# Optimization experiments

Measured on AMD Instinct MI355X. Metric: run time of the kernel, lower is better.

The kernel has to match this reference:

```python
import jax, jax.numpy as jnp
import numpy as np

N_NODES = 50000
N_EDGES = 800000
X_DIM, EDGE_DIM, H_DIM, HOUT = 92, 80, 128, 128
N_CONV = 3
N_GRAPHS = 256
BN_EPS = 1e-5


def setup_inputs() -> dict:
    key = jax.random.key(0)
    ks = jax.random.split(key, 16)
    x = jax.random.normal(ks[0], (N_NODES, X_DIM), dtype=jnp.float32)
    edge_index = jax.random.randint(ks[1], (2, N_EDGES), 0, N_NODES, dtype=jnp.int64)
    edge_attr = jax.random.normal(ks[2], (N_EDGES, EDGE_DIM), dtype=jnp.float32)
    batch = jnp.sort(jax.random.randint(ks[3], (N_NODES,), 0, N_GRAPHS, dtype=jnp.int64))
    s = 0.05
    embed_W = jax.random.normal(ks[4], (X_DIM, H_DIM), dtype=jnp.float32) * s
    embed_b = jnp.zeros((H_DIM,), jnp.float32)
    in_dim = 2 * H_DIM + EDGE_DIM
    conv_W = jax.random.normal(ks[5], (N_CONV, in_dim, 2 * H_DIM), dtype=jnp.float32) * s
    conv_b = jnp.zeros((N_CONV, 2 * H_DIM), jnp.float32)
    bn_i_g = jnp.ones((N_CONV, 2 * H_DIM), jnp.float32)
    bn_i_b = jnp.zeros((N_CONV, 2 * H_DIM), jnp.float32)
    bn_o_g = jnp.ones((N_CONV, H_DIM), jnp.float32)
    bn_o_b = jnp.zeros((N_CONV, H_DIM), jnp.float32)
    lin_W = jax.random.normal(ks[6], (H_DIM, HOUT), dtype=jnp.float32) * s
    lin_b = jnp.zeros((HOUT,), jnp.float32)
    out_W = jax.random.normal(ks[7], (HOUT, 1), dtype=jnp.float32) * s
    out_b = jnp.zeros((1,), jnp.float32)
    return {"x": x, "edge_index": edge_index, "edge_attr": edge_attr, "batch": batch,
            "embed_W": embed_W, "embed_b": embed_b, "conv_W": conv_W, "conv_b": conv_b,
            "bn_i_g": bn_i_g, "bn_i_b": bn_i_b, "bn_o_g": bn_o_g, "bn_o_b": bn_o_b,
            "lin_W": lin_W, "lin_b": lin_b, "out_W": out_W, "out_b": out_b}


def _bn(h, gamma, beta):
    # training-mode BatchNorm1d: biased batch statistics
    mu = jnp.mean(h, axis=0)
    var = jnp.mean(jnp.square(h - mu), axis=0)
    return (h - mu) * jax.lax.rsqrt(var + BN_EPS) * gamma + beta


def _cgconv(x, edge_index, edge_attr, W, b, gi, bi, go, bo):
    src, dst = edge_index[0], edge_index[1]
    msg = jnp.concatenate([x[src], edge_attr, x[dst]], axis=1)  # [E, 2h+e]
    msg = msg @ W + b                                           # [E, 2h]
    msg = _bn(msg, gi, bi)
    filt, core = jnp.split(msg, 2, axis=1)
    gated = jax.nn.sigmoid(filt) * jax.nn.softplus(core)        # [E, h]
    agg = jax.ops.segment_sum(gated, src, num_segments=N_NODES)  # [N, h]
    agg = _bn(agg, go, bo)
    return jax.nn.softplus(x + agg)


def reference(x, edge_index, edge_attr, batch, embed_W, embed_b, conv_W, conv_b,
              bn_i_g, bn_i_b, bn_o_g, bn_o_b, lin_W, lin_b, out_W, out_b):
    h = x @ embed_W + embed_b  # [N, h_dim]
    for i in range(N_CONV):
        h = _cgconv(h, edge_index, edge_attr, conv_W[i], conv_b[i],
                    bn_i_g[i], bn_i_b[i], bn_o_g[i], bn_o_b[i])
    # mean pooling per graph
    sums = jax.ops.segment_sum(h, batch, num_segments=N_GRAPHS)
    cnts = jax.ops.segment_sum(jnp.ones((h.shape[0],), h.dtype), batch, num_segments=N_GRAPHS)
    pooled = sums / jnp.maximum(cnts, 1.0)[:, None]  # [G, h_dim]
    g = jax.nn.softplus(pooled @ lin_W + lin_b)
    return g @ out_W + out_b  # [G, 1]
```

## Files before the change

kernel.cpp:

```cpp
#include <hip/hip_runtime.h>

constexpr int NN = 50000;
constexpr int NE = 800000;
constexpr int XD = 92;
constexpr int ED = 80;
constexpr int HD = 128;
constexpr int C2 = 256;
constexpr int IND = 336;
constexpr int NC = 3;
constexpr int NG = 256;
constexpr int NTILES = NE / 64;
constexpr int WSZ_L = 16 * 3 * 64 * 8;
constexpr int WNP_L = 16 * 4 * 64 * 8;

#define DINL __device__ __forceinline__

typedef __attribute__((ext_vector_type(8))) short bf16x8;
typedef __attribute__((ext_vector_type(4))) float f32x4;

DINL short f2bf(float f) {
  unsigned u = __float_as_uint(f);
  u = (u + 0x7fffu + ((u >> 16) & 1u)) >> 16;
  return (short)u;
}
DINL float bf2f(unsigned short u) { return __uint_as_float(((unsigned)u) << 16); }
DINL float bflo(unsigned u) { return __uint_as_float(u << 16); }
DINL float bfhi(unsigned u) { return __uint_as_float(u & 0xffff0000u); }
DINL float rcp_(float x) {
  float r;
  asm("v_rcp_f32 %0, %1" : "=v"(r) : "v"(x));
  return r;
}
DINL float softplusf_(float x) { return x > 20.f ? x : log1pf(__expf(x)); }
DINL float gate_(float f, float cr) {
  float e = __expf(-f);
  float s = rcp_(1.f + e);
  float t = __expf(cr);
  float l = (cr > 15.f) ? cr : __logf(1.f + t);
  return s * l;
}

template <int CTRL>
DINL int dpp_i(int old_, int src) {
  return __builtin_amdgcn_update_dpp(old_, src, CTRL, 0xF, 0xF, false);
}
template <int CTRL>
DINL float dpp_f(float old_, float src) {
  return __int_as_float(
      __builtin_amdgcn_update_dpp(__float_as_int(old_), __float_as_int(src), CTRL, 0xF, 0xF, false));
}
constexpr int SHR1 = 0x111, SHR2 = 0x112, SHR4 = 0x114, SHR8 = 0x118, SHL1 = 0x101;

__global__ __launch_bounds__(256) void k_embed(const float* __restrict__ x,
    const float* __restrict__ W, const float* __restrict__ b, float* __restrict__ h,
    unsigned short* __restrict__ hbf) {
  __shared__ float xs[2][XD];
  int t = threadIdx.x;
  int n0 = blockIdx.x * 2;
  for (int i = t; i < 2 * XD; i += 256) xs[i / XD][i % XD] = x[(size_t)n0 * XD + i];
  __syncthreads();
  int lo = t >> 7, c = t & 127;
  float acc = b[c];
  for (int k = 0; k < XD; ++k) acc = fmaf(xs[lo][k], W[k * HD + c], acc);
  h[(size_t)(n0 + lo) * HD + c] = acc;
  hbf[(size_t)(n0 + lo) * HD + c] = (unsigned short)f2bf(acc);
}

__global__ __launch_bounds__(256) void k_hist(const int* __restrict__ src,
                                              int* __restrict__ deg) {
  for (int e = blockIdx.x * 256 + threadIdx.x; e < NE; e += gridDim.x * 256)
    atomicAdd(&deg[src[e]], 1);
}

__global__ __launch_bounds__(1024) void k_scan(const int* __restrict__ deg,
                                               int* __restrict__ cursor) {
  __shared__ int sums[1024];
  int t = threadIdx.x;
  const int CH = 49;
  int b0 = t * CH;
  int s = 0;
  for (int i = 0; i < CH; ++i) {
    int idx = b0 + i;
    if (idx < NN) s += deg[idx];
  }
  sums[t] = s;
  __syncthreads();
  for (int off = 1; off < 1024; off <<= 1) {
    int v = (t >= off) ? sums[t - off] : 0;
    __syncthreads();
    sums[t] += v;
    __syncthreads();
  }
  int excl = (t == 0) ? 0 : sums[t - 1];
  for (int i = 0; i < CH; ++i) {
    int idx = b0 + i;
    if (idx < NN) {
      cursor[idx] = excl;
      excl += deg[idx];
    }
  }
}

__global__ __launch_bounds__(256) void k_scatter(const int* __restrict__ src,
    const int* __restrict__ dst, int* __restrict__ cursor, int* __restrict__ eid,
    int* __restrict__ ssort, int* __restrict__ dsort) {
  for (int e = blockIdx.x * 256 + threadIdx.x; e < NE; e += gridDim.x * 256) {
    int s = src[e];
    int pos = atomicAdd(&cursor[s], 1);
    eid[pos] = e;
    ssort[pos] = s;
    dsort[pos] = dst[e];
  }
}

__global__ __launch_bounds__(256) void k_wprep(const float* __restrict__ convW,
                                               unsigned short* __restrict__ Wswz) {
  int idx = blockIdx.x * 256 + threadIdx.x;
  if (idx >= NC * WSZ_L) return;
  int L = idx / WSZ_L;
  int rem = idx - L * WSZ_L;
  int mt = rem / 1536;
  int rem2 = rem - mt * 1536;
  int ks = rem2 >> 9;
  int lane = (rem2 >> 3) & 63;
  int j = rem2 & 7;
  int k = ks * 32 + (lane >> 4) * 8 + j;
  int m = mt * 16 + (lane & 15);
  float v = (k < ED) ? convW[(size_t)L * IND * C2 + (size_t)(HD + k) * C2 + m] : 0.f;
  Wswz[idx] = (unsigned short)f2bf(v);
}

__global__ __launch_bounds__(256) void k_wprep2(const float* __restrict__ convW,
                                                unsigned short* __restrict__ Wn) {
  int idx = blockIdx.x * 256 + threadIdx.x;
  if (idx >= NC * 2 * WNP_L) return;
  int Lh = idx >> 15;
  int L = Lh >> 1, half = Lh & 1;
  int rem = idx & 32767;
  int mt = rem >> 11;
  int rem2 = rem & 2047;
  int ks = rem2 >> 9;
  int lane = (rem2 >> 3) & 63;
  int j = rem2 & 7;
  int k = ks * 32 + (lane >> 4) * 8 + j;
  int m = mt * 16 + (lane & 15);
  int row = (half ? 208 : 0) + k;
  Wn[idx] = (unsigned short)f2bf(convW[(size_t)L * IND * C2 + (size_t)row * C2 + m]);
}

__global__ __launch_bounds__(256) void k_nodeproj2(const unsigned short* __restrict__ hbf,
    const unsigned short* __restrict__ Wn, int L,
    ushort4* __restrict__ P1, ushort4* __restrict__ P3) {
  __shared__ bf16x8 hls[1024];
  __shared__ ushort4 outls[4096];
  int t = threadIdx.x, w = t >> 6, l = t & 63, g = l >> 4, c = l & 15;
  int n0 = blockIdx.x * 64;
  int half = blockIdx.y;
  for (int i = t; i < 1024; i += 256) {
    int node = i >> 4, chunk = i & 15;
    int gn = n0 + node;
    if (gn >= NN) gn = NN - 1;
    bf16x8 v = *(const bf16x8*)(hbf + (size_t)gn * HD + chunk * 8);
    hls[node * 16 + (chunk ^ (node & 7))] = v;
  }
  __syncthreads();
  const bf16x8* Wf = (const bf16x8*)(Wn + ((size_t)(L * 2 + half)) * WNP_L);
  bf16x8 af[4][4];
#pragma unroll
  for (int mm = 0; mm < 4; ++mm)
#pragma unroll
    for (int ks = 0; ks < 4; ++ks) af[mm][ks] = Wf[((w * 4 + mm) * 4 + ks) * 64 + l];
  f32x4 acc[4][4];
#pragma unroll
  for (int mm = 0; mm < 4; ++mm)
#pragma unroll
    for (int nt = 0; nt < 4; ++nt)
#pragma unroll
      for (int i = 0; i < 4; ++i) acc[mm][nt][i] = 0.f;
#pragma unroll
  for (int nt = 0; nt < 4; ++nt) {
    int node = nt * 16 + c;
#pragma unroll
    for (int ks = 0; ks < 4; ++ks) {
      bf16x8 b = hls[node * 16 + ((4 * ks + g) ^ (node & 7))];
#pragma unroll
      for (int mm = 0; mm < 4; ++mm)
        acc[mm][nt] = __builtin_amdgcn_mfma_f32_16x16x32_bf16(af[mm][ks], b, acc[mm][nt], 0, 0, 0);
    }
  }
  __syncthreads();
#pragma unroll
  for (int mm = 0; mm < 4; ++mm) {
    int mt = w * 4 + mm;
    int wE = (mt & 7) >> 1;
    int mE = (mt & 1) | ((mt >> 3) << 1);
    int slot = (wE * 4 + g) * 4 + mE;
#pragma unroll
    for (int nt = 0; nt < 4; ++nt) {
      int node = nt * 16 + c;
      ushort4 st;
      st.x = (unsigned short)f2bf(acc[mm][nt][0]);
      st.y = (unsigned short)f2bf(acc[mm][nt][1]);
      st.z = (unsigned short)f2bf(acc[mm][nt][2]);
      st.w = (unsigned short)f2bf(acc[mm][nt][3]);
      outls[node * 64 + (slot ^ ((node & 7) << 3))] = st;
    }
  }
  __syncthreads();
  ushort4* P = half ? P3 : P1;
  for (int i = t; i < 4096; i += 256) {
    int row = i >> 6, slot = i & 63;
    int gn = n0 + row;
    if (gn < NN) P[(size_t)gn * 64 + slot] = outls[row * 64 + (slot ^ ((row & 7) << 3))];
  }
}

__global__ __launch_bounds__(256) void k_eaprep(const int* __restrict__ eid,
    const float* __restrict__ ea, bf16x8* __restrict__ eaf) {
  int idx = blockIdx.x * 256 + threadIdx.x;
  if (idx >= NTILES * 768) return;
  int tile = idx / 768;
  int r = idx - tile * 768;
  int fr = r >> 6, l = r & 63;
  int nt = fr / 3, ks = fr - 3 * nt;
  int c = l & 15, g = l >> 4;
  int k0 = ks * 32 + g * 8;
  bf16x8 v;
  if (k0 < ED) {
    int e = eid[tile * 64 + nt * 16 + c];
    const float* p = ea + (size_t)e * ED + k0;
    float4 x0 = *(const float4*)p;
    float4 x1 = *(const float4*)(p + 4);
    v[0] = f2bf(x0.x); v[1] = f2bf(x0.y); v[2] = f2bf(x0.z); v[3] = f2bf(x0.w);
    v[4] = f2bf(x1.x); v[5] = f2bf(x1.y); v[6] = f2bf(x1.z); v[7] = f2bf(x1.w);
  } else {
#pragma unroll
    for (int j = 0; j < 8; ++j) v[j] = 0;
  }
  eaf[idx] = v;
}

__global__ __launch_bounds__(256, 2) void k_estat2(
    const int* __restrict__ ssort, const int* __restrict__ dsort,
    const bf16x8* __restrict__ eaf, const unsigned short* __restrict__ Wswz,
    const uint4* __restrict__ P1p, const uint4* __restrict__ P3p,
    ushort4* __restrict__ msgc, float* __restrict__ stats) {
  int t = threadIdx.x;
  int w = t >> 6, l = t & 63;
  int g = l >> 4, c = l & 15;
  int mtg[4] = {2 * w, 2 * w + 1, 2 * w + 8, 2 * w + 9};
  int gi2 = (w * 4 + g) * 2;
  const bf16x8* Wf = (const bf16x8*)Wswz;
  bf16x8 af[4][3];
#pragma unroll
  for (int m = 0; m < 4; ++m)
#pragma unroll
    for (int ks = 0; ks < 3; ++ks) af[m][ks] = Wf[(mtg[m] * 3 + ks) * 64 + l];
  f32x4 ssum[4], ssq[4];
#pragma unroll
  for (int m = 0; m < 4; ++m)
#pragma unroll
    for (int i = 0; i < 4; ++i) { ssum[m][i] = 0.f; ssq[m][i] = 0.f; }

  const int stride = gridDim.x;
  int tile = blockIdx.x;
  int s_[4], d_[4];
  if (tile < NTILES) {
#pragma unroll
    for (int nt = 0; nt < 4; ++nt) {
      s_[nt] = ssort[tile * 64 + nt * 16 + c];
      d_[nt] = dsort[tile * 64 + nt * 16 + c];
    }
  }
  for (; tile < NTILES; tile += stride) {
    bf16x8 b_[12];
    const bf16x8* bp = eaf + (size_t)tile * 768 + l;
#pragma unroll
    for (int fr = 0; fr < 12; ++fr) b_[fr] = bp[fr * 64];
    uint4 q1a[4], q1b[4], q3a[4], q3b[4];
#pragma unroll
    for (int nt = 0; nt < 4; ++nt) {
      const uint4* p1 = P1p + (size_t)s_[nt] * 32 + gi2;
      const uint4* p3 = P3p + (size_t)d_[nt] * 32 + gi2;
      q1a[nt] = p1[0];
      q1b[nt] = p1[1];
      q3a[nt] = p3[0];
      q3b[nt] = p3[1];
    }
    int sn[4], dn[4];
    int tn = tile + stride;
    if (tn < NTILES) {
#pragma unroll
      for (int nt = 0; nt < 4; ++nt) {
        sn[nt] = ssort[tn * 64 + nt * 16 + c];
        dn[nt] = dsort[tn * 64 + nt * 16 + c];
      }
    } else {
#pragma unroll
      for (int nt = 0; nt < 4; ++nt) { sn[nt] = 0; dn[nt] = 0; }
    }
#pragma unroll
    for (int nt = 0; nt < 4; ++nt) {
      f32x4 acc[4];
#pragma unroll
      for (int m = 0; m < 4; ++m) {
        acc[m][0] = 0.f; acc[m][1] = 0.f; acc[m][2] = 0.f; acc[m][3] = 0.f;
      }
#pragma unroll
      for (int ks = 0; ks < 3; ++ks)
#pragma unroll
        for (int m = 0; m < 4; ++m)
          acc[m] = __builtin_amdgcn_mfma_f32_16x16x32_bf16(af[m][ks], b_[nt * 3 + ks],
                                                           acc[m], 0, 0, 0);
      unsigned pu1[8] = {q1a[nt].x, q1a[nt].y, q1a[nt].z, q1a[nt].w,
                         q1b[nt].x, q1b[nt].y, q1b[nt].z, q1b[nt].w};
      unsigned pu3[8] = {q3a[nt].x, q3a[nt].y, q3a[nt].z, q3a[nt].w,
                         q3b[nt].x, q3b[nt].y, q3b[nt].z, q3b[nt].w};
#pragma unroll
      for (int m = 0; m < 4; ++m) {
        unsigned a1 = pu1[2 * m], b1 = pu1[2 * m + 1];
        unsigned a3 = pu3[2 * m], b3 = pu3[2 * m + 1];
        f32x4 ms;
        ms[0] = acc[m][0] + bflo(a1) + bflo(a3);
        ms[1] = acc[m][1] + bfhi(a1) + bfhi(a3);
        ms[2] = acc[m][2] + bflo(b1) + bflo(b3);
        ms[3] = acc[m][3] + bfhi(b1) + bfhi(b3);
#pragma unroll
        for (int i = 0; i < 4; ++i) {
          ssum[m][i] += ms[i];
          ssq[m][i] = fmaf(ms[i], ms[i], ssq[m][i]);
        }
        ushort4 st;
        st.x = (unsigned short)f2bf(ms[0]);
        st.y = (unsigned short)f2bf(ms[1]);
        st.z = (unsigned short)f2bf(ms[2]);
        st.w = (unsigned short)f2bf(ms[3]);
        msgc[(((size_t)tile * 4 + nt) * 16 + w * 4 + m) * 64 + l] = st;
      }
    }
#pragma unroll
    for (int nt = 0; nt < 4; ++nt) { s_[nt] = sn[nt]; d_[nt] = dn[nt]; }
  }
#pragma unroll
  for (int off = 1; off < 16; off <<= 1)
#pragma unroll
    for (int m = 0; m < 4; ++m)
#pragma unroll
      for (int i = 0; i < 4; ++i) {
        ssum[m][i] += __shfl_xor(ssum[m][i], off, 16);
        ssq[m][i] += __shfl_xor(ssq[m][i], off, 16);
      }
  if (c == 0) {
#pragma unroll
    for (int m = 0; m < 4; ++m)
#pragma unroll
      for (int i = 0; i < 4; ++i) {
        int ch = mtg[m] * 16 + 4 * g + i;
        atomicAdd(&stats[ch], ssum[m][i]);
        atomicAdd(&stats[C2 + ch], ssq[m][i]);
      }
  }
}

__global__ __launch_bounds__(256) void k_apply2(
    const int* __restrict__ ssort, const ushort4* __restrict__ msgc,
    const float* __restrict__ st, const float* __restrict__ gammaI,
    const float* __restrict__ betaI, float* __restrict__ agg) {
  int t = threadIdx.x;
  int w = t >> 6, l = t & 63;
  int g = l >> 4, c = l & 15;
  int mtg[4] = {2 * w, 2 * w + 1, 2 * w + 8, 2 * w + 9};
  f32x4 sc4[4], sh4[4];
#pragma unroll
  for (int m = 0; m < 4; ++m)
#pragma unroll
    for (int i = 0; i < 4; ++i) {
      int ch = mtg[m] * 16 + 4 * g + i;
      float mean = st[ch] * (1.f / NE);
      float var = st[C2 + ch] * (1.f / NE) - mean * mean;
      float scv = gammaI[ch] * rsqrtf(var + 1e-5f);
      sc4[m][i] = scv;
      sh4[m][i] = betaI[ch] - mean * scv;
    }
  const int stride = gridDim.x;
  int tile = blockIdx.x;
  if (tile >= NTILES) return;
  int s_[4];
  ushort4 mw[4][4];
#pragma unroll
  for (int nt = 0; nt < 4; ++nt) {
    s_[nt] = ssort[tile * 64 + nt * 16 + c];
#pragma unroll
    for (int m = 0; m < 4; ++m)
      mw[nt][m] = msgc[(((size_t)tile * 4 + nt) * 16 + w * 4 + m) * 64 + l];
  }
  for (; tile < NTILES; tile += stride) {
    int tn = tile + stride;
    int ti = (tn < NTILES) ? tn : tile;
    int sn[4];
    ushort4 mwn[4][4];
#pragma unroll
    for (int nt = 0; nt < 4; ++nt) {
      sn[nt] = ssort[ti * 64 + nt * 16 + c];
#pragma unroll
      for (int m = 0; m < 4; ++m)
        mwn[nt][m] = msgc[(((size_t)ti * 4 + nt) * 16 + w * 4 + m) * 64 + l];
    }
#pragma unroll
    for (int nt = 0; nt < 4; ++nt) {
      int sv = s_[nt];
      int ps = dpp_i<SHR1>(-1, sv);
      int hp = (ps != sv) ? c : 0;
      hp = max(hp, dpp_i<SHR1>(0, hp));
      hp = max(hp, dpp_i<SHR2>(0, hp));
      hp = max(hp, dpp_i<SHR4>(0, hp));
      hp = max(hp, dpp_i<SHR8>(0, hp));
      int ns = dpp_i<SHL1>(-1, sv);
      bool tail = (ns != sv);
      bool g1 = (c - 1) >= hp, g2 = (c - 2) >= hp, g4 = (c - 4) >= hp, g8 = (c - 8) >= hp;
      f32x4 v4[4];
#pragma unroll
      for (int m = 0; m < 4; ++m) {
        v4[m][0] = fmaf(bf2f(mw[nt][m].x), sc4[m][0], sh4[m][0]);
        v4[m][1] = fmaf(bf2f(mw[nt][m].y), sc4[m][1], sh4[m][1]);
        v4[m][2] = fmaf(bf2f(mw[nt][m].z), sc4[m][2], sh4[m][2]);
        v4[m][3] = fmaf(bf2f(mw[nt][m].w), sc4[m][3], sh4[m][3]);
      }
      float gg_[8];
#pragma unroll
      for (int p = 0; p < 2; ++p)
#pragma unroll
        for (int i = 0; i < 4; ++i)
          gg_[p * 4 + i] = gate_(v4[p][i], v4[p + 2][i]);
#pragma unroll
      for (int q = 0; q < 8; ++q) {
        float tv;
        tv = dpp_f<SHR1>(0.f, gg_[q]); gg_[q] += g1 ? tv : 0.f;
        tv = dpp_f<SHR2>(0.f, gg_[q]); gg_[q] += g2 ? tv : 0.f;
        tv = dpp_f<SHR4>(0.f, gg_[q]); gg_[q] += g4 ? tv : 0.f;
        tv = dpp_f<SHR8>(0.f, gg_[q]); gg_[q] += g8 ? tv : 0.f;
      }
      if (tail) {
#pragma unroll
        for (int p = 0; p < 2; ++p)
#pragma unroll
          for (int i = 0; i < 4; ++i)
            atomicAdd(&agg[(size_t)sv * HD + mtg[p] * 16 + 4 * g + i], gg_[p * 4 + i]);
      }
    }
#pragma unroll
    for (int nt = 0; nt < 4; ++nt) {
      s_[nt] = sn[nt];
#pragma unroll
      for (int m = 0; m < 4; ++m) mw[nt][m] = mwn[nt][m];
    }
  }
}

__global__ __launch_bounds__(256) void k_aggstat(const float* __restrict__ agg,
                                                 float* __restrict__ stats) {
  int t = threadIdx.x;
  int c = t & 127, half = t >> 7;
  float s = 0.f, sq = 0.f;
  for (int n = blockIdx.x * 2 + half; n < NN; n += gridDim.x * 2) {
    float v = agg[(size_t)n * HD + c];
    s += v;
    sq = fmaf(v, v, sq);
  }
  __shared__ float shs[2][128], shq[2][128];
  shs[half][c] = s;
  shq[half][c] = sq;
  __syncthreads();
  if (t < 128) {
    atomicAdd(&stats[c], shs[0][c] + shs[1][c]);
    atomicAdd(&stats[128 + c], shq[0][c] + shq[1][c]);
  }
}

__global__ __launch_bounds__(256) void k_update(const float* __restrict__ h,
    const float* __restrict__ agg, const float* __restrict__ st_o,
    const float* __restrict__ bog, const float* __restrict__ bob,
    float* __restrict__ hn, unsigned short* __restrict__ hbf) {
  int stride = gridDim.x * 256;
  for (int i = blockIdx.x * 256 + threadIdx.x; i < NN * HD; i += stride) {
    int c = i & 127;
    float mean = st_o[c] * (1.f / NN);
    float var = st_o[128 + c] * (1.f / NN) - mean * mean;
    float scv = bog[c] * rsqrtf(var + 1e-5f);
    float shv = bob[c] - mean * scv;
    float v = h[i] + fmaf(agg[i], scv, shv);
    float r = softplusf_(v);
    hn[i] = r;
    hbf[i] = (unsigned short)f2bf(r);
  }
}

__global__ __launch_bounds__(256) void k_pool(const float* __restrict__ h,
    const int* __restrict__ batch, float* __restrict__ psum, int* __restrict__ pcnt) {
  int stride = gridDim.x * 256;
  for (int i = blockIdx.x * 256 + threadIdx.x; i < NN * HD; i += stride) {
    int n = i >> 7, c = i & 127;
    int g = batch[n];
    atomicAdd(&psum[g * HD + c], h[i]);
    if (c == 0) atomicAdd(&pcnt[g], 1);
  }
}

__global__ __launch_bounds__(128) void k_head(const float* __restrict__ psum,
    const int* __restrict__ pcnt, const float* __restrict__ linW,
    const float* __restrict__ linb, const float* __restrict__ outW,
    const float* __restrict__ outb, float* __restrict__ out) {
  __shared__ float pl[HD];
  __shared__ float red[2];
  int g = blockIdx.x, t = threadIdx.x;
  float cnt = fmaxf((float)pcnt[g], 1.f);
  pl[t] = psum[g * HD + t] / cnt;
  __syncthreads();
  float acc = linb[t];
  for (int k = 0; k < HD; ++k) acc = fmaf(pl[k], linW[k * HD + t], acc);
  float term = softplusf_(acc) * outW[t];
#pragma unroll
  for (int off = 32; off > 0; off >>= 1) term += __shfl_down(term, off, 64);
  if ((t & 63) == 0) red[t >> 6] = term;
  __syncthreads();
  if (t == 0) out[g] = red[0] + red[1] + outb[0];
}

extern "C" void kernel_launch(void* const* d_in, const int* in_sizes, int n_in,
                              void* d_out, int out_size, void* d_ws, size_t ws_size,
                              hipStream_t stream) {
  const float* x = (const float*)d_in[0];
  const int* ei = (const int*)d_in[1];
  const float* ea = (const float*)d_in[2];
  const int* batch = (const int*)d_in[3];
  const float* embW = (const float*)d_in[4];
  const float* embb = (const float*)d_in[5];
  const float* convW = (const float*)d_in[6];
  const float* big = (const float*)d_in[8];
  const float* bib = (const float*)d_in[9];
  const float* bog = (const float*)d_in[10];
  const float* bob = (const float*)d_in[11];
  const float* linW = (const float*)d_in[12];
  const float* linb = (const float*)d_in[13];
  const float* outW = (const float*)d_in[14];
  const float* outb = (const float*)d_in[15];
  float* out = (float*)d_out;

  float* wsf = (float*)d_ws;
  size_t off = 0;
  auto alloc = [&](size_t n) {
    float* p = wsf + off;
    off += (n + 3) & ~(size_t)3;
    return p;
  };
  float* h0 = alloc((size_t)NN * HD);
  float* h1 = alloc((size_t)NN * HD);
  unsigned short* hbf = (unsigned short*)alloc((size_t)NN * HD / 2);
  ushort4* P1b = (ushort4*)alloc((size_t)NN * C2 / 2);
  ushort4* P3b = (ushort4*)alloc((size_t)NN * C2 / 2);
  float* agg = alloc((size_t)NN * HD);
  float* st_i = alloc(2 * C2);
  float* st_o = alloc(2 * HD);
  float* psum = alloc((size_t)NG * HD);
  int* pcnt = (int*)alloc(NG);
  int* deg = (int*)alloc(NN);
  int* cursor = (int*)alloc(NN);
  int* eid = (int*)alloc(NE);
  int* ssort = (int*)alloc(NE);
  int* dsort = (int*)alloc(NE);
  unsigned short* Wswz = (unsigned short*)alloc((NC * WSZ_L + 1) / 2);
  unsigned short* Wn = (unsigned short*)alloc((NC * 2 * WNP_L + 1) / 2);
  bf16x8* eaf = (bf16x8*)alloc((size_t)NTILES * 768 * 4);
  ushort4* msgc = (ushort4*)alloc((size_t)NE * C2 / 2);

  const int* srcp = ei;
  const int* dstp = ei + NE;

  hipMemsetAsync(deg, 0, NN * sizeof(int), stream);
  k_hist<<<2048, 256, 0, stream>>>(srcp, deg);
  k_scan<<<1, 1024, 0, stream>>>(deg, cursor);
  k_scatter<<<2048, 256, 0, stream>>>(srcp, dstp, cursor, eid, ssort, dsort);

  k_wprep<<<(NC * WSZ_L + 255) / 256, 256, 0, stream>>>(convW, Wswz);
  k_wprep2<<<(NC * 2 * WNP_L + 255) / 256, 256, 0, stream>>>(convW, Wn);
  k_eaprep<<<(NTILES * 768 + 255) / 256, 256, 0, stream>>>(eid, ea, eaf);
  k_embed<<<NN / 2, 256, 0, stream>>>(x, embW, embb, h0, hbf);

  float* hc = h0;
  float* hn = h1;
  for (int L = 0; L < NC; ++L) {
    const unsigned short* Wl = Wswz + (size_t)L * WSZ_L;
    hipMemsetAsync(st_i, 0, 2 * C2 * sizeof(float), stream);
    hipMemsetAsync(st_o, 0, 2 * HD * sizeof(float), stream);
    hipMemsetAsync(agg, 0, (size_t)NN * HD * sizeof(float), stream);

    dim3 npgrid((NN + 63) / 64, 2);
    k_nodeproj2<<<npgrid, 256, 0, stream>>>(hbf, Wn, L, P1b, P3b);
    k_estat2<<<2500, 256, 0, stream>>>(ssort, dsort, eaf, Wl,
        (const uint4*)P1b, (const uint4*)P3b, msgc, st_i);
    k_apply2<<<2500, 256, 0, stream>>>(ssort, msgc, st_i, big + L * C2, bib + L * C2, agg);
    k_aggstat<<<512, 256, 0, stream>>>(agg, st_o);
    k_update<<<2048, 256, 0, stream>>>(hc, agg, st_o, bog + L * HD, bob + L * HD, hn, hbf);
    float* tmp = hc; hc = hn; hn = tmp;
  }

  hipMemsetAsync(psum, 0, (size_t)NG * HD * sizeof(float), stream);
  hipMemsetAsync(pcnt, 0, NG * sizeof(int), stream);
  k_pool<<<2048, 256, 0, stream>>>(hc, batch, psum, pcnt);
  k_head<<<NG, 128, 0, stream>>>(psum, pcnt, linW, linb, outW, outb, out);
}
```

Before: 2.236 ms.

## Split edge-stat kernel work into half-channel units across twice as many blocks

```diff
diff --git a/kernel.cpp b/kernel.cpp
--- a/kernel.cpp
+++ b/kernel.cpp
@@ -248,76 +248,70 @@
   int t = threadIdx.x;
   int w = t >> 6, l = t & 63;
   int g = l >> 4, c = l & 15;
-  int mtg[4] = {2 * w, 2 * w + 1, 2 * w + 8, 2 * w + 9};
-  int gi2 = (w * 4 + g) * 2;
+  const int stride = gridDim.x;
+  int unit = blockIdx.x;
+  int h = unit & 1;
+  int mtg[2] = {2 * w + 8 * h, 2 * w + 1 + 8 * h};
+  int giq = (w * 4 + g) * 2 + h;
   const bf16x8* Wf = (const bf16x8*)Wswz;
-  bf16x8 af[4][3];
-#pragma unroll
-  for (int m = 0; m < 4; ++m)
+  bf16x8 af[2][3];
+#pragma unroll
+  for (int m = 0; m < 2; ++m)
 #pragma unroll
     for (int ks = 0; ks < 3; ++ks) af[m][ks] = Wf[(mtg[m] * 3 + ks) * 64 + l];
-  f32x4 ssum[4], ssq[4];
-#pragma unroll
-  for (int m = 0; m < 4; ++m)
+  f32x4 ssum[2], ssq[2];
+#pragma unroll
+  for (int m = 0; m < 2; ++m)
 #pragma unroll
     for (int i = 0; i < 4; ++i) { ssum[m][i] = 0.f; ssq[m][i] = 0.f; }
 
-  const int stride = gridDim.x;
-  int tile = blockIdx.x;
+  const int NUNITS = 2 * NTILES;
   int s_[4], d_[4];
-  if (tile < NTILES) {
-#pragma unroll
-    for (int nt = 0; nt < 4; ++nt) {
-      s_[nt] = ssort[tile * 64 + nt * 16 + c];
-      d_[nt] = dsort[tile * 64 + nt * 16 + c];
-    }
-  }
-  for (; tile < NTILES; tile += stride) {
+  {
+    int tile0 = unit >> 1;
+#pragma unroll
+    for (int nt = 0; nt < 4; ++nt) {
+      s_[nt] = ssort[tile0 * 64 + nt * 16 + c];
+      d_[nt] = dsort[tile0 * 64 + nt * 16 + c];
+    }
+  }
+  for (; unit < NUNITS; unit += stride) {
+    int tile = unit >> 1;
     bf16x8 b_[12];
     const bf16x8* bp = eaf + (size_t)tile * 768 + l;
 #pragma unroll
     for (int fr = 0; fr < 12; ++fr) b_[fr] = bp[fr * 64];
-    uint4 q1a[4], q1b[4], q3a[4], q3b[4];
-#pragma unroll
-    for (int nt = 0; nt < 4; ++nt) {
-      const uint4* p1 = P1p + (size_t)s_[nt] * 32 + gi2;
-      const uint4* p3 = P3p + (size_t)d_[nt] * 32 + gi2;
-      q1a[nt] = p1[0];
-      q1b[nt] = p1[1];
-      q3a[nt] = p3[0];
-      q3b[nt] = p3[1];
+    uint4 q1[4], q3[4];
+#pragma unroll
+    for (int nt = 0; nt < 4; ++nt) {
+      q1[nt] = P1p[(size_t)s_[nt] * 32 + giq];
+      q3[nt] = P3p[(size_t)d_[nt] * 32 + giq];
     }
     int sn[4], dn[4];
-    int tn = tile + stride;
-    if (tn < NTILES) {
-#pragma unroll
-      for (int nt = 0; nt < 4; ++nt) {
-        sn[nt] = ssort[tn * 64 + nt * 16 + c];
-        dn[nt] = dsort[tn * 64 + nt * 16 + c];
-      }
-    } else {
-#pragma unroll
-      for (int nt = 0; nt < 4; ++nt) { sn[nt] = 0; dn[nt] = 0; }
-    }
-#pragma unroll
-    for (int nt = 0; nt < 4; ++nt) {
-      f32x4 acc[4];
-#pragma unroll
-      for (int m = 0; m < 4; ++m) {
+    int un = unit + stride;
+    int tin = (un < NUNITS) ? (un >> 1) : (unit >> 1);
+#pragma unroll
+    for (int nt = 0; nt < 4; ++nt) {
+      sn[nt] = ssort[tin * 64 + nt * 16 + c];
+      dn[nt] = dsort[tin * 64 + nt * 16 + c];
+    }
+#pragma unroll
+    for (int nt = 0; nt < 4; ++nt) {
+      f32x4 acc[2];
+#pragma unroll
+      for (int m = 0; m < 2; ++m) {
         acc[m][0] = 0.f; acc[m][1] = 0.f; acc[m][2] = 0.f; acc[m][3] = 0.f;
       }
 #pragma unroll
       for (int ks = 0; ks < 3; ++ks)
 #pragma unroll
-        for (int m = 0; m < 4; ++m)
+        for (int m = 0; m < 2; ++m)
           acc[m] = __builtin_amdgcn_mfma_f32_16x16x32_bf16(af[m][ks], b_[nt * 3 + ks],
                                                            acc[m], 0, 0, 0);
-      unsigned pu1[8] = {q1a[nt].x, q1a[nt].y, q1a[nt].z, q1a[nt].w,
-                         q1b[nt].x, q1b[nt].y, q1b[nt].z, q1b[nt].w};
-      unsigned pu3[8] = {q3a[nt].x, q3a[nt].y, q3a[nt].z, q3a[nt].w,
-                         q3b[nt].x, q3b[nt].y, q3b[nt].z, q3b[nt].w};
-#pragma unroll
-      for (int m = 0; m < 4; ++m) {
+      unsigned pu1[4] = {q1[nt].x, q1[nt].y, q1[nt].z, q1[nt].w};
+      unsigned pu3[4] = {q3[nt].x, q3[nt].y, q3[nt].z, q3[nt].w};
+#pragma unroll
+      for (int m = 0; m < 2; ++m) {
         unsigned a1 = pu1[2 * m], b1 = pu1[2 * m + 1];
         unsigned a3 = pu3[2 * m], b3 = pu3[2 * m + 1];
         f32x4 ms;
@@ -335,7 +329,7 @@
         st.y = (unsigned short)f2bf(ms[1]);
         st.z = (unsigned short)f2bf(ms[2]);
         st.w = (unsigned short)f2bf(ms[3]);
-        msgc[(((size_t)tile * 4 + nt) * 16 + w * 4 + m) * 64 + l] = st;
+        msgc[(((size_t)tile * 4 + nt) * 16 + w * 4 + 2 * h + m) * 64 + l] = st;
       }
     }
 #pragma unroll
@@ -344,7 +338,7 @@
 #pragma unroll
   for (int off = 1; off < 16; off <<= 1)
 #pragma unroll
-    for (int m = 0; m < 4; ++m)
+    for (int m = 0; m < 2; ++m)
 #pragma unroll
       for (int i = 0; i < 4; ++i) {
         ssum[m][i] += __shfl_xor(ssum[m][i], off, 16);
@@ -352,7 +346,7 @@
       }
   if (c == 0) {
 #pragma unroll
-    for (int m = 0; m < 4; ++m)
+    for (int m = 0; m < 2; ++m)
 #pragma unroll
       for (int i = 0; i < 4; ++i) {
         int ch = mtg[m] * 16 + 4 * g + i;
@@ -596,7 +590,7 @@
 
     dim3 npgrid((NN + 63) / 64, 2);
     k_nodeproj2<<<npgrid, 256, 0, stream>>>(hbf, Wn, L, P1b, P3b);
-    k_estat2<<<2500, 256, 0, stream>>>(ssort, dsort, eaf, Wl,
+    k_estat2<<<5000, 256, 0, stream>>>(ssort, dsort, eaf, Wl,
         (const uint4*)P1b, (const uint4*)P3b, msgc, st_i);
     k_apply2<<<2500, 256, 0, stream>>>(ssort, msgc, st_i, big + L * C2, bib + L * C2, agg);
     k_aggstat<<<512, 256, 0, stream>>>(agg, st_o);
```

Measured after the change: 2.462 ms. 1.1x slower.

## Recompute edge messages in apply pass instead of storing bf16 intermediate

Applied to the files above, without the earlier changes.

```diff
diff --git a/kernel.cpp b/kernel.cpp
--- a/kernel.cpp
+++ b/kernel.cpp
@@ -240,11 +240,11 @@
   eaf[idx] = v;
 }
 
-__global__ __launch_bounds__(256, 2) void k_estat2(
+__global__ __launch_bounds__(256, 2) void k_estat3(
     const int* __restrict__ ssort, const int* __restrict__ dsort,
     const bf16x8* __restrict__ eaf, const unsigned short* __restrict__ Wswz,
     const uint4* __restrict__ P1p, const uint4* __restrict__ P3p,
-    ushort4* __restrict__ msgc, float* __restrict__ stats) {
+    float* __restrict__ stats) {
   int t = threadIdx.x;
   int w = t >> 6, l = t & 63;
   int g = l >> 4, c = l & 15;
@@ -330,12 +330,6 @@
           ssum[m][i] += ms[i];
           ssq[m][i] = fmaf(ms[i], ms[i], ssq[m][i]);
         }
-        ushort4 st;
-        st.x = (unsigned short)f2bf(ms[0]);
-        st.y = (unsigned short)f2bf(ms[1]);
-        st.z = (unsigned short)f2bf(ms[2]);
-        st.w = (unsigned short)f2bf(ms[3]);
-        msgc[(((size_t)tile * 4 + nt) * 16 + w * 4 + m) * 64 + l] = st;
       }
     }
 #pragma unroll
@@ -362,14 +356,23 @@
   }
 }
 
-__global__ __launch_bounds__(256) void k_apply2(
-    const int* __restrict__ ssort, const ushort4* __restrict__ msgc,
+__global__ __launch_bounds__(256, 2) void k_apply3(
+    const int* __restrict__ ssort, const int* __restrict__ dsort,
+    const bf16x8* __restrict__ eaf, const unsigned short* __restrict__ Wswz,
+    const uint4* __restrict__ P1p, const uint4* __restrict__ P3p,
     const float* __restrict__ st, const float* __restrict__ gammaI,
     const float* __restrict__ betaI, float* __restrict__ agg) {
   int t = threadIdx.x;
   int w = t >> 6, l = t & 63;
   int g = l >> 4, c = l & 15;
   int mtg[4] = {2 * w, 2 * w + 1, 2 * w + 8, 2 * w + 9};
+  int gi2 = (w * 4 + g) * 2;
+  const bf16x8* Wf = (const bf16x8*)Wswz;
+  bf16x8 af[4][3];
+#pragma unroll
+  for (int m = 0; m < 4; ++m)
+#pragma unroll
+    for (int ks = 0; ks < 3; ++ks) af[m][ks] = Wf[(mtg[m] * 3 + ks) * 64 + l];
   f32x4 sc4[4], sh4[4];
 #pragma unroll
   for (int m = 0; m < 4; ++m)
@@ -382,32 +385,71 @@
       sc4[m][i] = scv;
       sh4[m][i] = betaI[ch] - mean * scv;
     }
+
   const int stride = gridDim.x;
   int tile = blockIdx.x;
-  if (tile >= NTILES) return;
-  int s_[4];
-  ushort4 mw[4][4];
-#pragma unroll
-  for (int nt = 0; nt < 4; ++nt) {
-    s_[nt] = ssort[tile * 64 + nt * 16 + c];
-#pragma unroll
-    for (int m = 0; m < 4; ++m)
-      mw[nt][m] = msgc[(((size_t)tile * 4 + nt) * 16 + w * 4 + m) * 64 + l];
+  int s_[4], d_[4];
+  if (tile < NTILES) {
+#pragma unroll
+    for (int nt = 0; nt < 4; ++nt) {
+      s_[nt] = ssort[tile * 64 + nt * 16 + c];
+      d_[nt] = dsort[tile * 64 + nt * 16 + c];
+    }
   }
   for (; tile < NTILES; tile += stride) {
+    bf16x8 b_[12];
+    const bf16x8* bp = eaf + (size_t)tile * 768 + l;
+#pragma unroll
+    for (int fr = 0; fr < 12; ++fr) b_[fr] = bp[fr * 64];
+    uint4 q1a[4], q1b[4], q3a[4], q3b[4];
+#pragma unroll
+    for (int nt = 0; nt < 4; ++nt) {
+      const uint4* p1 = P1p + (size_t)s_[nt] * 32 + gi2;
+      const uint4* p3 = P3p + (size_t)d_[nt] * 32 + gi2;
+      q1a[nt] = p1[0];
+      q1b[nt] = p1[1];
+      q3a[nt] = p3[0];
+      q3b[nt] = p3[1];
+    }
+    int sn[4], dn[4];
     int tn = tile + stride;
-    int ti = (tn < NTILES) ? tn : tile;
-    int sn[4];
-    ushort4 mwn[4][4];
+    if (tn < NTILES) {
+#pragma unroll
+      for (int nt = 0; nt < 4; ++nt) {
+        sn[nt] = ssort[tn * 64 + nt * 16 + c];
+        dn[nt] = dsort[tn * 64 + nt * 16 + c];
+      }
+    } else {
+#pragma unroll
+      for (int nt = 0; nt < 4; ++nt) { sn[nt] = 0; dn[nt] = 0; }
+    }
 #pragma unroll
     for (int nt = 0; nt < 4; ++nt) {
-      sn[nt] = ssort[ti * 64 + nt * 16 + c];
-#pragma unroll
-      for (int m = 0; m < 4; ++m)
-        mwn[nt][m] = msgc[(((size_t)ti * 4 + nt) * 16 + w * 4 + m) * 64 + l];
-    }
-#pragma unroll
-    for (int nt = 0; nt < 4; ++nt) {
+      f32x4 acc[4];
+#pragma unroll
+      for (int m = 0; m < 4; ++m) {
+        acc[m][0] = 0.f; acc[m][1] = 0.f; acc[m][2] = 0.f; acc[m][3] = 0.f;
+      }
+#pragma unroll
+      for (int ks = 0; ks < 3; ++ks)
+#pragma unroll
+        for (int m = 0; m < 4; ++m)
+          acc[m] = __builtin_amdgcn_mfma_f32_16x16x32_bf16(af[m][ks], b_[nt * 3 + ks],
+                                                           acc[m], 0, 0, 0);
+      unsigned pu1[8] = {q1a[nt].x, q1a[nt].y, q1a[nt].z, q1a[nt].w,
+                         q1b[nt].x, q1b[nt].y, q1b[nt].z, q1b[nt].w};
+      unsigned pu3[8] = {q3a[nt].x, q3a[nt].y, q3a[nt].z, q3a[nt].w,
+                         q3b[nt].x, q3b[nt].y, q3b[nt].z, q3b[nt].w};
+      f32x4 v4[4];
+#pragma unroll
+      for (int m = 0; m < 4; ++m) {
+        unsigned a1 = pu1[2 * m], b1 = pu1[2 * m + 1];
+        unsigned a3 = pu3[2 * m], b3 = pu3[2 * m + 1];
+        v4[m][0] = fmaf(acc[m][0] + bflo(a1) + bflo(a3), sc4[m][0], sh4[m][0]);
+        v4[m][1] = fmaf(acc[m][1] + bfhi(a1) + bfhi(a3), sc4[m][1], sh4[m][1]);
+        v4[m][2] = fmaf(acc[m][2] + bflo(b1) + bflo(b3), sc4[m][2], sh4[m][2]);
+        v4[m][3] = fmaf(acc[m][3] + bfhi(b1) + bfhi(b3), sc4[m][3], sh4[m][3]);
+      }
       int sv = s_[nt];
       int ps = dpp_i<SHR1>(-1, sv);
       int hp = (ps != sv) ? c : 0;
@@ -418,14 +460,6 @@
       int ns = dpp_i<SHL1>(-1, sv);
       bool tail = (ns != sv);
       bool g1 = (c - 1) >= hp, g2 = (c - 2) >= hp, g4 = (c - 4) >= hp, g8 = (c - 8) >= hp;
-      f32x4 v4[4];
-#pragma unroll
-      for (int m = 0; m < 4; ++m) {
-        v4[m][0] = fmaf(bf2f(mw[nt][m].x), sc4[m][0], sh4[m][0]);
-        v4[m][1] = fmaf(bf2f(mw[nt][m].y), sc4[m][1], sh4[m][1]);
-        v4[m][2] = fmaf(bf2f(mw[nt][m].z), sc4[m][2], sh4[m][2]);
-        v4[m][3] = fmaf(bf2f(mw[nt][m].w), sc4[m][3], sh4[m][3]);
-      }
       float gg_[8];
 #pragma unroll
       for (int p = 0; p < 2; ++p)
@@ -449,11 +483,7 @@
       }
     }
 #pragma unroll
-    for (int nt = 0; nt < 4; ++nt) {
-      s_[nt] = sn[nt];
-#pragma unroll
-      for (int m = 0; m < 4; ++m) mw[nt][m] = mwn[nt][m];
-    }
+    for (int nt = 0; nt < 4; ++nt) { s_[nt] = sn[nt]; d_[nt] = dn[nt]; }
   }
 }
 
@@ -571,7 +601,6 @@
   unsigned short* Wswz = (unsigned short*)alloc((NC * WSZ_L + 1) / 2);
   unsigned short* Wn = (unsigned short*)alloc((NC * 2 * WNP_L + 1) / 2);
   bf16x8* eaf = (bf16x8*)alloc((size_t)NTILES * 768 * 4);
-  ushort4* msgc = (ushort4*)alloc((size_t)NE * C2 / 2);
 
   const int* srcp = ei;
   const int* dstp = ei + NE;
@@ -596,9 +625,10 @@
 
     dim3 npgrid((NN + 63) / 64, 2);
     k_nodeproj2<<<npgrid, 256, 0, stream>>>(hbf, Wn, L, P1b, P3b);
-    k_estat2<<<2500, 256, 0, stream>>>(ssort, dsort, eaf, Wl,
-        (const uint4*)P1b, (const uint4*)P3b, msgc, st_i);
-    k_apply2<<<2500, 256, 0, stream>>>(ssort, msgc, st_i, big + L * C2, bib + L * C2, agg);
+    k_estat3<<<2500, 256, 0, stream>>>(ssort, dsort, eaf, Wl,
+        (const uint4*)P1b, (const uint4*)P3b, st_i);
+    k_apply3<<<2500, 256, 0, stream>>>(ssort, dsort, eaf, Wl,
+        (const uint4*)P1b, (const uint4*)P3b, st_i, big + L * C2, bib + L * C2, agg);
     k_aggstat<<<512, 256, 0, stream>>>(agg, st_o);
     k_update<<<2048, 256, 0, stream>>>(hc, agg, st_o, bog + L * HD, bob + L * HD, hn, hbf);
     float* tmp = hc; hc = hn; hn = tmp;
```

Measured after the change: 2.419 ms. +8.2%, slower.
